# Optimization experiments

Hardware: AMD Instinct MI355X
Metric: run time of the kernel (lower is better)

Reference implementation:

```python
import jax, jax.numpy as jnp
import numpy as np

B, S = 2, 2048          # sequences, tokens per sequence (equal-length varlen batch)
HK, HV = 16, 32         # key heads, value heads (GQA ratio 2)
DK = DV = 128           # head dims (asserted equal in module)
K = 4                   # causal conv kernel width
QKV = HK * DK * 2 + HV * DV  # 8192
CHUNK = 64
EPS = 1e-6


def _causal_conv1d_silu(x, w):
    # x: [B, S, QKV], w: [QKV, K] depthwise causal conv (zero history), then SiLU
    xp = jnp.pad(x, ((0, 0), (K - 1, 0), (0, 0)))
    y = xp[:, 0:S, :] * w[:, 0]
    for j in range(1, K):
        y = y + xp[:, j:j + S, :] * w[:, j]
    return jax.nn.silu(y)


def _l2norm(x):
    return x * jax.lax.rsqrt(jnp.sum(x * x, axis=-1, keepdims=True) + EPS)


def _gdn_forward(mixed_qkv, b, a, conv_weights, dt_bias, alog):
    x = mixed_qkv.reshape(B, S, QKV)
    y = _causal_conv1d_silu(x, conv_weights)
    q = _l2norm(y[..., :HK * DK].reshape(B, S, HK, DK))
    k = _l2norm(y[..., HK * DK:2 * HK * DK].reshape(B, S, HK, DK))
    v = y[..., 2 * HK * DK:].reshape(B, S, HV, DV)
    # fused_gdn_gating: g = -exp(A_log) * softplus(a + dt_bias), beta = sigmoid(b)
    g = (-jnp.exp(alog) * jax.nn.softplus(a + dt_bias)).reshape(B, S, HV)
    beta = jax.nn.sigmoid(b).reshape(B, S, HV)
    r = HV // HK  # GQA: repeat q/k heads to match value heads
    q = jnp.repeat(q, r, axis=2)
    k = jnp.repeat(k, r, axis=2)
    scale = DK ** -0.5

    def tm(t):  # [B,S,...] -> [S//CHUNK, CHUNK, B, ...] (time-major, chunked)
        tt = jnp.moveaxis(t, 1, 0)
        return tt.reshape((S // CHUNK, CHUNK) + tt.shape[1:])

    qs, ks, vs, gs, bs = tm(q), tm(k), tm(v), tm(g), tm(beta)

    def inner(St, inp):
        # St: [B,HV,DK,DV] gated delta-rule state
        qt, kt, vt, gt, bt = inp
        St = St * jnp.exp(gt)[..., None, None]
        pred = jnp.einsum('bhk,bhkv->bhv', kt, St)
        St = St + kt[..., None] * (bt[..., None] * (vt - pred))[..., None, :]
        o = jnp.einsum('bhk,bhkv->bhv', qt * scale, St)
        return St, o

    @jax.checkpoint
    def chunk_step(St, cin):
        return jax.lax.scan(inner, St, cin)

    S0 = jnp.zeros((B, HV, DK, DV), mixed_qkv.dtype)
    _, o = jax.lax.scan(chunk_step, S0, (qs, ks, vs, gs, bs))
    o = o.reshape(S, B, HV, DV)           # [S,B,HV,DV]
    return jnp.moveaxis(o, 0, 1).reshape(B * S, HV, DV)


def setup_inputs() -> dict:
    ks = jax.random.split(jax.random.key(0), 6)
    return {
        'mixed_qkv': jax.random.normal(ks[0], (B * S, QKV), jnp.float32),
        'b': jax.random.normal(ks[1], (B * S, HV), jnp.float32),
        'a': jax.random.normal(ks[2], (B * S, HV), jnp.float32),
        'conv_weights': 0.25 * jax.random.normal(ks[3], (QKV, K), jnp.float32),
        'dt_bias': jax.random.normal(ks[4], (HV,), jnp.float32),
        'alog': jax.random.normal(ks[5], (HV,), jnp.float32),
        'cu_seqlens': jnp.arange(B + 1, dtype=jnp.int32) * S,
    }


def reference(mixed_qkv, b, a, conv_weights, dt_bias, alog, cu_seqlens):
    # cu_seqlens encodes equal-length sequences [0, S, 2S]; math uses the [B,S] reshape
    return _gdn_forward(mixed_qkv, b, a, conv_weights, dt_bias, alog)
```

## Files before the change

### kernel.cpp

```cpp
#include <hip/hip_runtime.h>
#include <hip/hip_bf16.h>


#define B_    2
#define S_    2048
#define HK_   16
#define HV_   32
#define DK_   128
#define QKV_  8192
#define EPS_  1e-6f
#define SCALE_ 0.08838834764831845f
#define CH_   16
#define NCH_  (S_ / CH_)

#define AS_GLOBAL __attribute__((address_space(1)))
#define AS_LDS    __attribute__((address_space(3)))

__device__ __forceinline__ void gload16(const float* src, float* dst) {
    __builtin_amdgcn_global_load_lds((const AS_GLOBAL void*)src,
                                     (AS_LDS void*)dst, 16, 0, 0);
}
__device__ __forceinline__ void gload4(const float* src, float* dst) {
    __builtin_amdgcn_global_load_lds((const AS_GLOBAL void*)src,
                                     (AS_LDS void*)dst, 4, 0, 0);
}

__device__ __forceinline__ float red8(float x) {
    int t;
    t = __builtin_amdgcn_update_dpp(0, __float_as_int(x), 0xB1, 0xF, 0xF, true);
    x += __int_as_float(t);
    t = __builtin_amdgcn_update_dpp(0, __float_as_int(x), 0x4E, 0xF, 0xF, true);
    x += __int_as_float(t);
    t = __builtin_amdgcn_update_dpp(0, __float_as_int(x), 0x141, 0xF, 0xF, true);
    x += __int_as_float(t);
    return x;
}

__global__ __launch_bounds__(256)
void preproc_kernel(const float* __restrict__ x, const float* __restrict__ w,
                    float* __restrict__ Y)
{
    const int seg = blockIdx.x;
    const int bt0 = blockIdx.y * 4;
    const int t0  = bt0 & (S_ - 1);
    const int tid = threadIdx.x;
    const int c0  = seg * 2048 + tid * 8;

    float4 w4[8];
#pragma unroll
    for (int i = 0; i < 8; ++i)
        w4[i] = *reinterpret_cast<const float4*>(&w[(c0 + i) * 4]);

    float h0[8], h1[8], h2[8], cur[8], y[8];

#pragma unroll
    for (int i = 0; i < 8; ++i) { h0[i] = 0.f; h1[i] = 0.f; h2[i] = 0.f; }
    if (t0 >= 3) {
        const float* r0 = &x[(size_t)(bt0 - 3) * QKV_ + c0];
        const float* r1 = &x[(size_t)(bt0 - 2) * QKV_ + c0];
        const float* r2 = &x[(size_t)(bt0 - 1) * QKV_ + c0];
#pragma unroll
        for (int i4 = 0; i4 < 2; ++i4) {
            const float4 a = *reinterpret_cast<const float4*>(r0 + i4 * 4);
            const float4 b = *reinterpret_cast<const float4*>(r1 + i4 * 4);
            const float4 c = *reinterpret_cast<const float4*>(r2 + i4 * 4);
            h0[4*i4+0]=a.x; h0[4*i4+1]=a.y; h0[4*i4+2]=a.z; h0[4*i4+3]=a.w;
            h1[4*i4+0]=b.x; h1[4*i4+1]=b.y; h1[4*i4+2]=b.z; h1[4*i4+3]=b.w;
            h2[4*i4+0]=c.x; h2[4*i4+1]=c.y; h2[4*i4+2]=c.z; h2[4*i4+3]=c.w;
        }
    }

#pragma unroll
    for (int tt = 0; tt < 4; ++tt) {
        const float* rc = &x[(size_t)(bt0 + tt) * QKV_ + c0];
#pragma unroll
        for (int i4 = 0; i4 < 2; ++i4) {
            const float4 a = *reinterpret_cast<const float4*>(rc + i4 * 4);
            cur[4*i4+0]=a.x; cur[4*i4+1]=a.y; cur[4*i4+2]=a.z; cur[4*i4+3]=a.w;
        }
#pragma unroll
        for (int i = 0; i < 8; ++i) {
            float v = h0[i]*w4[i].x + h1[i]*w4[i].y + h2[i]*w4[i].z + cur[i]*w4[i].w;
            y[i] = v / (1.f + expf(-v));
        }
        if (seg < 2) {
            float s = 0.f;
#pragma unroll
            for (int i = 0; i < 8; ++i) s += y[i] * y[i];
#pragma unroll
            for (int off = 8; off >= 1; off >>= 1)
                s += __shfl_xor(s, off, 64);
            float rn = rsqrtf(s + EPS_);
            if (seg == 0) rn *= SCALE_;
#pragma unroll
            for (int i = 0; i < 8; ++i) y[i] *= rn;
        }
        float4* dst = reinterpret_cast<float4*>(&Y[(size_t)(bt0 + tt) * QKV_ + c0]);
        dst[0] = make_float4(y[0], y[1], y[2], y[3]);
        dst[1] = make_float4(y[4], y[5], y[6], y[7]);
#pragma unroll
        for (int i = 0; i < 8; ++i) { h0[i] = h1[i]; h1[i] = h2[i]; h2[i] = cur[i]; }
    }
}

__global__ __launch_bounds__(256)
void gating_kernel(const float* __restrict__ bin, const float* __restrict__ ain,
                   const float* __restrict__ dtb, const float* __restrict__ alg,
                   float2* __restrict__ GB)
{
    const int i = blockIdx.x * 256 + threadIdx.x;
    if (i >= B_ * S_ * HV_) return;
    const int h = i & (HV_ - 1);
    const float av = ain[i] + dtb[h];
    const float sp = (av > 20.f) ? av : log1pf(expf(av));
    GB[i] = make_float2(expf(-expf(alg[h]) * sp), 1.f / (1.f + expf(-bin[i])));
}

__device__ __forceinline__ void lds_load_kqv(const float* __restrict__ Kt,
                                             const float* __restrict__ Qt,
                                             const float* __restrict__ Vt,
                                             int kh, int vloc, int sw,
                                             float (&kf)[16], float (&qf)[16],
                                             float& vv)
{
#pragma unroll
    for (int r = 0; r < 4; ++r) {
        const int idx = r ^ sw;
        const float4 kq = *reinterpret_cast<const float4*>(Kt + kh * 16 + idx * 4);
        const float4 qq = *reinterpret_cast<const float4*>(Qt + kh * 16 + idx * 4);
        kf[4*r+0]=kq.x; kf[4*r+1]=kq.y; kf[4*r+2]=kq.z; kf[4*r+3]=kq.w;
        qf[4*r+0]=qq.x; qf[4*r+1]=qq.y; qf[4*r+2]=qq.z; qf[4*r+3]=qq.w;
    }
    vv = Vt[vloc];
}

__device__ __forceinline__ void step_pair(float (&S)[16],
    const float (&k0)[16], const float (&q0)[16], float v0,
    const float (&k1)[16], const float (&q1)[16], float v1,
    float4 g,
    int kh, float* __restrict__ o0p, float* __restrict__ o1p)
{
    float a0 = 0.f, a1 = 0.f, cc = 0.f, u0 = 0.f,
          u1 = 0.f, w00 = 0.f, w10 = 0.f, w11 = 0.f;
#pragma unroll
    for (int j = 0; j < 16; ++j) {
        a0  += k0[j] * S[j];
        a1  += k1[j] * S[j];
        cc  += k1[j] * k0[j];
        u0  += q0[j] * S[j];
        u1  += q1[j] * S[j];
        w00 += q0[j] * k0[j];
        w10 += q1[j] * k0[j];
        w11 += q1[j] * k1[j];
    }
    a0 = red8(a0);  a1 = red8(a1);  cc = red8(cc);  u0 = red8(u0);
    u1 = red8(u1);  w00 = red8(w00); w10 = red8(w10); w11 = red8(w11);

    const float eg0 = g.x, b0 = g.y, eg1 = g.z, b1 = g.w;
    const float d0   = b0 * (v0 - eg0 * a0);
    const float eg01 = eg0 * eg1;
    const float p1   = fmaf(eg1 * cc, d0, eg01 * a1);
    const float d1   = b1 * (v1 - p1);
    const float o0   = fmaf(w00, d0, eg0 * u0);
    const float o1   = fmaf(w11, d1, fmaf(eg1 * w10, d0, eg01 * u1));
    const float bb   = eg1 * d0;
#pragma unroll
    for (int j = 0; j < 16; ++j)
        S[j] = fmaf(eg01, S[j], fmaf(bb, k0[j], d1 * k1[j]));

    if (kh == 0) { *o0p = o0; *o1p = o1; }
}

__global__ __launch_bounds__(64, 1)
void recur_kernel(const float* __restrict__ Y, const float2* __restrict__ GB,
                  float* __restrict__ out)
{
    const int h    = blockIdx.x;
    const int b    = blockIdx.y;
    const int vs   = blockIdx.z;
    const int hk   = h >> 1;
    const int lane = threadIdx.x;
    const int kh   = lane & 7;
    const int vloc = lane >> 3;
    const int sw   = kh >> 1;

    const int qoff0 = hk * DK_;
    const int koff0 = 2048 + hk * DK_;
    const int voff0 = 4096 + h * DK_ + vs * 8;

    __shared__ __align__(16) float Ksm[2][CH_][128];
    __shared__ __align__(16) float Qsm[2][CH_][128];
    __shared__ __align__(16) float Vsm[2][CH_ * 8];
    __shared__ __align__(16) float Gsm[2][64];

    const float* rowBase = Y + (size_t)(b * S_) * QKV_;
    const float* gflat   = (const float*)(GB + (size_t)(b * S_) * HV_ + h);
    float* obase = out + ((size_t)(b * S_) * HV_ + h) * (size_t)DK_ + vs * 8 + vloc;

    const int tk = lane >> 5;
    const int gr = lane & 31;

    auto issue_chunk = [&](int t0, int bsel) {
#pragma unroll
        for (int i = 0; i < 8; ++i)
            gload16(rowBase + (size_t)(t0 + 2 * i + tk) * QKV_ + koff0 + gr * 4,
                    &Ksm[bsel][2 * i][0]);
#pragma unroll
        for (int i = 0; i < 8; ++i)
            gload16(rowBase + (size_t)(t0 + 2 * i + tk) * QKV_ + qoff0 + gr * 4,
                    &Qsm[bsel][2 * i][0]);
#pragma unroll
        for (int i = 0; i < 2; ++i)
            gload4(rowBase + (size_t)(t0 + i * 8 + (lane >> 3)) * QKV_
                           + voff0 + (lane & 7),
                   &Vsm[bsel][i * 64]);
        gload4(gflat + (size_t)(t0 + ((lane >> 1) & 15)) * (HV_ * 2) + (lane & 1),
               &Gsm[bsel][0]);
    };

    float S[16];
#pragma unroll
    for (int j = 0; j < 16; ++j) S[j] = 0.f;

    issue_chunk(0, 0);
    issue_chunk(CH_, 1);
    asm volatile("s_waitcnt vmcnt(19)" ::: "memory");

    float k0A[16], q0A[16], k1A[16], q1A[16], v0A, v1A;
    float k0B[16], q0B[16], k1B[16], q1B[16], v0B, v1B;
    float4 gA, gB4;

    for (int c = 0; c < NCH_; ++c) {
        const int bsel = c & 1;
        const int t0   = c * CH_;
        const float (*Kc)[128] = Ksm[bsel];
        const float (*Qc)[128] = Qsm[bsel];
        const float* Vc = Vsm[bsel];
        const float* Gc = Gsm[bsel];

        lds_load_kqv(Kc[0], Qc[0], Vc + 0,  kh, vloc, sw, k0A, q0A, v0A);
        lds_load_kqv(Kc[1], Qc[1], Vc + 8,  kh, vloc, sw, k1A, q1A, v1A);
        gA = *reinterpret_cast<const float4*>(Gc + 0);
        lds_load_kqv(Kc[2], Qc[2], Vc + 16, kh, vloc, sw, k0B, q0B, v0B);
        lds_load_kqv(Kc[3], Qc[3], Vc + 24, kh, vloc, sw, k1B, q1B, v1B);
        gB4 = *reinterpret_cast<const float4*>(Gc + 4);

#pragma unroll
        for (int pp = 0; pp < CH_ / 2; pp += 2) {
            step_pair(S, k0A, q0A, v0A, k1A, q1A, v1A, gA, kh,
                      obase + (size_t)(t0 + 2 * pp)     * (HV_ * DK_),
                      obase + (size_t)(t0 + 2 * pp + 1) * (HV_ * DK_));
            if (pp + 2 < CH_ / 2) {
                const int ta = 2 * (pp + 2);
                lds_load_kqv(Kc[ta],     Qc[ta],     Vc + ta * 8,
                             kh, vloc, sw, k0A, q0A, v0A);
                lds_load_kqv(Kc[ta + 1], Qc[ta + 1], Vc + (ta + 1) * 8,
                             kh, vloc, sw, k1A, q1A, v1A);
                gA = *reinterpret_cast<const float4*>(Gc + 2 * ta);
            }
            __builtin_amdgcn_sched_barrier(0);
            step_pair(S, k0B, q0B, v0B, k1B, q1B, v1B, gB4, kh,
                      obase + (size_t)(t0 + 2 * pp + 2) * (HV_ * DK_),
                      obase + (size_t)(t0 + 2 * pp + 3) * (HV_ * DK_));
            if (pp + 3 < CH_ / 2) {
                const int tb = 2 * (pp + 3);
                lds_load_kqv(Kc[tb],     Qc[tb],     Vc + tb * 8,
                             kh, vloc, sw, k0B, q0B, v0B);
                lds_load_kqv(Kc[tb + 1], Qc[tb + 1], Vc + (tb + 1) * 8,
                             kh, vloc, sw, k1B, q1B, v1B);
                gB4 = *reinterpret_cast<const float4*>(Gc + 2 * tb);
            }
        }

        const int tn = (c + 2 < NCH_) ? (c + 2) * CH_ : (NCH_ - 1) * CH_;
        issue_chunk(tn, bsel);
        asm volatile("s_waitcnt vmcnt(35)" ::: "memory");
    }
}

__global__ __launch_bounds__(128)
void gdn_prefill_fallback(const float* __restrict__ xqkv, const float* __restrict__ bin,
                          const float* __restrict__ ain, const float* __restrict__ wconv,
                          const float* __restrict__ dtb, const float* __restrict__ alg,
                          float* __restrict__ out)
{
    const int h = blockIdx.x, b = blockIdx.y;
    const int hk = h >> 1;
    const int tid = threadIdx.x, lane = tid & 63, wid = tid >> 6;
    __shared__ __align__(16) float ks[DK_];
    __shared__ __align__(16) float qs[DK_];
    __shared__ float redq[2], redk[2];
    const int qc = hk * DK_ + tid, kc = HK_ * DK_ + hk * DK_ + tid,
              vc = 2 * HK_ * DK_ + h * DK_ + tid;
    float wq[4], wk[4], wv[4];
#pragma unroll
    for (int j = 0; j < 4; ++j) {
        wq[j] = wconv[qc*4+j]; wk[j] = wconv[kc*4+j]; wv[j] = wconv[vc*4+j];
    }
    const float nea = -expf(alg[h]), dbi = dtb[h];
    float hq0=0,hq1=0,hq2=0,hk0=0,hk1=0,hk2=0,hv0=0,hv1=0,hv2=0;
    float Sr[DK_];
#pragma unroll
    for (int k = 0; k < DK_; ++k) Sr[k] = 0.f;
    const size_t row0 = (size_t)b * S_;
    for (int t = 0; t < S_; ++t) {
        const size_t row = row0 + t, xb = row * QKV_;
        const float xq = xqkv[xb+qc], xk = xqkv[xb+kc], xv = xqkv[xb+vc];
        float yq = hq0*wq[0]+hq1*wq[1]+hq2*wq[2]+xq*wq[3];
        float yk = hk0*wk[0]+hk1*wk[1]+hk2*wk[2]+xk*wk[3];
        float yv = hv0*wv[0]+hv1*wv[1]+hv2*wv[2]+xv*wv[3];
        hq0=hq1;hq1=hq2;hq2=xq; hk0=hk1;hk1=hk2;hk2=xk; hv0=hv1;hv1=hv2;hv2=xv;
        yq = yq/(1.f+expf(-yq)); yk = yk/(1.f+expf(-yk)); yv = yv/(1.f+expf(-yv));
        float sq = yq*yq, sk = yk*yk;
#pragma unroll
        for (int off = 32; off >= 1; off >>= 1) {
            sq += __shfl_xor(sq, off, 64); sk += __shfl_xor(sk, off, 64);
        }
        if (lane == 0) { redq[wid] = sq; redk[wid] = sk; }
        __syncthreads();
        const float qn = yq * rsqrtf(redq[0]+redq[1]+EPS_) * SCALE_;
        const float kn = yk * rsqrtf(redk[0]+redk[1]+EPS_);
        ks[tid] = kn; qs[tid] = qn;
        const size_t rab = row * HV_ + h;
        const float av = ain[rab] + dbi;
        const float sp = (av > 20.f) ? av : log1pf(expf(av));
        const float eg = expf(nea * sp);
        const float beta = 1.f/(1.f+expf(-bin[rab]));
        __syncthreads();
        float pred = 0.f;
#pragma unroll
        for (int k4 = 0; k4 < DK_/4; ++k4) {
            const float4 kv = *reinterpret_cast<const float4*>(&ks[k4*4]);
            float s;
            s = Sr[4*k4+0]*eg; Sr[4*k4+0]=s; pred += kv.x*s;
            s = Sr[4*k4+1]*eg; Sr[4*k4+1]=s; pred += kv.y*s;
            s = Sr[4*k4+2]*eg; Sr[4*k4+2]=s; pred += kv.z*s;
            s = Sr[4*k4+3]*eg; Sr[4*k4+3]=s; pred += kv.w*s;
        }
        const float delta = beta * (yv - pred);
        float o = 0.f;
#pragma unroll
        for (int k4 = 0; k4 < DK_/4; ++k4) {
            const float4 kv = *reinterpret_cast<const float4*>(&ks[k4*4]);
            const float4 qv = *reinterpret_cast<const float4*>(&qs[k4*4]);
            float s;
            s = Sr[4*k4+0]+kv.x*delta; Sr[4*k4+0]=s; o += qv.x*s;
            s = Sr[4*k4+1]+kv.y*delta; Sr[4*k4+1]=s; o += qv.y*s;
            s = Sr[4*k4+2]+kv.z*delta; Sr[4*k4+2]=s; o += qv.z*s;
            s = Sr[4*k4+3]+kv.w*delta; Sr[4*k4+3]=s; o += qv.w*s;
        }
        out[rab * DK_ + tid] = o;
    }
}

extern "C" void kernel_launch(void* const* d_in, const int* in_sizes, int n_in,
                              void* d_out, int out_size, void* d_ws, size_t ws_size,
                              hipStream_t stream) {
    const float* xqkv  = (const float*)d_in[0];
    const float* bin   = (const float*)d_in[1];
    const float* ain   = (const float*)d_in[2];
    const float* wconv = (const float*)d_in[3];
    const float* dtb   = (const float*)d_in[4];
    const float* alg   = (const float*)d_in[5];
    float* out = (float*)d_out;

    const size_t Y_BYTES = (size_t)B_ * S_ * QKV_ * 4;
    const size_t G_BYTES = (size_t)B_ * S_ * HV_ * 8;
    const size_t NEEDED  = Y_BYTES + G_BYTES;

    if (ws_size >= NEEDED) {
        float*  Y  = (float*)d_ws;
        float2* GB = (float2*)((char*)d_ws + Y_BYTES);

        preproc_kernel<<<dim3(4, B_ * S_ / 4), 256, 0, stream>>>(xqkv, wconv, Y);
        gating_kernel<<<dim3((B_ * S_ * HV_ + 255) / 256), 256, 0, stream>>>(
            bin, ain, dtb, alg, GB);
        recur_kernel<<<dim3(HV_, B_, 16), 64, 0, stream>>>(Y, GB, out);
    } else {
        gdn_prefill_fallback<<<dim3(HV_, B_), 128, 0, stream>>>(
            xqkv, bin, ain, wconv, dtb, alg, out);
    }
}
```

Baseline: 827.2 us.

## Split recurrence state across 16 lanes and double the value-column grid

Each wavefront now owns 4 value columns instead of 8, with 16 lanes each holding 8 key rows of the state instead of 8 lanes holding 16. The grid's z dimension doubles to 32, the chunk size drops to 8, and the DPP reduction gains a fourth stage to cover 16 lanes. The aim is to shorten the serial per-token dependency chain and put more wavefronts on the GPU, since the recurrence is latency-bound. In exchange, every block reloads the full K/Q rows for fewer outputs, doubling redundant loads, and each dot product pays an extra reduction step.

Result: slower. 1.116 ms (+34.9%).

```diff
diff --git a/kernel.cpp b/kernel.cpp
--- a/kernel.cpp
+++ b/kernel.cpp
@@ -10,7 +10,7 @@
 #define QKV_  8192
 #define EPS_  1e-6f
 #define SCALE_ 0.08838834764831845f
-#define CH_   16
+#define CH_   8
 #define NCH_  (S_ / CH_)
 
 #define AS_GLOBAL __attribute__((address_space(1)))
@@ -25,7 +25,7 @@
                                      (AS_LDS void*)dst, 4, 0, 0);
 }
 
-__device__ __forceinline__ float red8(float x) {
+__device__ __forceinline__ float red16(float x) {
     int t;
     t = __builtin_amdgcn_update_dpp(0, __float_as_int(x), 0xB1, 0xF, 0xF, true);
     x += __int_as_float(t);
@@ -33,6 +33,8 @@
     x += __int_as_float(t);
     t = __builtin_amdgcn_update_dpp(0, __float_as_int(x), 0x141, 0xF, 0xF, true);
     x += __int_as_float(t);
+    t = __builtin_amdgcn_update_dpp(0, __float_as_int(x), 0x140, 0xF, 0xF, true);
+    x += __int_as_float(t);
     return x;
 }
 
@@ -116,34 +118,34 @@
     GB[i] = make_float2(expf(-expf(alg[h]) * sp), 1.f / (1.f + expf(-bin[i])));
 }
 
-__device__ __forceinline__ void lds_load_kqv(const float* __restrict__ Kt,
-                                             const float* __restrict__ Qt,
-                                             const float* __restrict__ Vt,
-                                             int kh, int vloc, int sw,
-                                             float (&kf)[16], float (&qf)[16],
-                                             float& vv)
-{
-#pragma unroll
-    for (int r = 0; r < 4; ++r) {
+__device__ __forceinline__ void lds_load_kqv8(const float* __restrict__ Kt,
+                                              const float* __restrict__ Qt,
+                                              const float* __restrict__ Vt,
+                                              int kh16, int vloc, int sw,
+                                              float (&kf)[8], float (&qf)[8],
+                                              float& vv)
+{
+#pragma unroll
+    for (int r = 0; r < 2; ++r) {
         const int idx = r ^ sw;
-        const float4 kq = *reinterpret_cast<const float4*>(Kt + kh * 16 + idx * 4);
-        const float4 qq = *reinterpret_cast<const float4*>(Qt + kh * 16 + idx * 4);
+        const float4 kq = *reinterpret_cast<const float4*>(Kt + kh16 * 8 + idx * 4);
+        const float4 qq = *reinterpret_cast<const float4*>(Qt + kh16 * 8 + idx * 4);
         kf[4*r+0]=kq.x; kf[4*r+1]=kq.y; kf[4*r+2]=kq.z; kf[4*r+3]=kq.w;
         qf[4*r+0]=qq.x; qf[4*r+1]=qq.y; qf[4*r+2]=qq.z; qf[4*r+3]=qq.w;
     }
     vv = Vt[vloc];
 }
 
-__device__ __forceinline__ void step_pair(float (&S)[16],
-    const float (&k0)[16], const float (&q0)[16], float v0,
-    const float (&k1)[16], const float (&q1)[16], float v1,
+__device__ __forceinline__ void step_pair(float (&S)[8],
+    const float (&k0)[8], const float (&q0)[8], float v0,
+    const float (&k1)[8], const float (&q1)[8], float v1,
     float4 g,
-    int kh, float* __restrict__ o0p, float* __restrict__ o1p)
+    int kh16, float* __restrict__ o0p, float* __restrict__ o1p)
 {
     float a0 = 0.f, a1 = 0.f, cc = 0.f, u0 = 0.f,
           u1 = 0.f, w00 = 0.f, w10 = 0.f, w11 = 0.f;
 #pragma unroll
-    for (int j = 0; j < 16; ++j) {
+    for (int j = 0; j < 8; ++j) {
         a0  += k0[j] * S[j];
         a1  += k1[j] * S[j];
         cc  += k1[j] * k0[j];
@@ -153,8 +155,8 @@
         w10 += q1[j] * k0[j];
         w11 += q1[j] * k1[j];
     }
-    a0 = red8(a0);  a1 = red8(a1);  cc = red8(cc);  u0 = red8(u0);
-    u1 = red8(u1);  w00 = red8(w00); w10 = red8(w10); w11 = red8(w11);
+    a0 = red16(a0);  a1 = red16(a1);  cc = red16(cc);  u0 = red16(u0);
+    u1 = red16(u1);  w00 = red16(w00); w10 = red16(w10); w11 = red16(w11);
 
     const float eg0 = g.x, b0 = g.y, eg1 = g.z, b1 = g.w;
     const float d0   = b0 * (v0 - eg0 * a0);
@@ -165,13 +167,13 @@
     const float o1   = fmaf(w11, d1, fmaf(eg1 * w10, d0, eg01 * u1));
     const float bb   = eg1 * d0;
 #pragma unroll
-    for (int j = 0; j < 16; ++j)
+    for (int j = 0; j < 8; ++j)
         S[j] = fmaf(eg01, S[j], fmaf(bb, k0[j], d1 * k1[j]));
 
-    if (kh == 0) { *o0p = o0; *o1p = o1; }
-}
-
-__global__ __launch_bounds__(64, 1)
+    if (kh16 == 0) { *o0p = o0; *o1p = o1; }
+}
+
+__global__ __launch_bounds__(64, 2)
 void recur_kernel(const float* __restrict__ Y, const float2* __restrict__ GB,
                   float* __restrict__ out)
 {
@@ -180,54 +182,51 @@
     const int vs   = blockIdx.z;
     const int hk   = h >> 1;
     const int lane = threadIdx.x;
-    const int kh   = lane & 7;
-    const int vloc = lane >> 3;
-    const int sw   = kh >> 1;
+    const int kh16 = lane & 15;
+    const int vloc = lane >> 4;
+    const int sw   = (kh16 >> 2) & 1;
 
     const int qoff0 = hk * DK_;
     const int koff0 = 2048 + hk * DK_;
-    const int voff0 = 4096 + h * DK_ + vs * 8;
+    const int voff0 = 4096 + h * DK_ + vs * 4;
 
     __shared__ __align__(16) float Ksm[2][CH_][128];
     __shared__ __align__(16) float Qsm[2][CH_][128];
-    __shared__ __align__(16) float Vsm[2][CH_ * 8];
+    __shared__ __align__(16) float Vsm[2][64];
     __shared__ __align__(16) float Gsm[2][64];
 
     const float* rowBase = Y + (size_t)(b * S_) * QKV_;
     const float* gflat   = (const float*)(GB + (size_t)(b * S_) * HV_ + h);
-    float* obase = out + ((size_t)(b * S_) * HV_ + h) * (size_t)DK_ + vs * 8 + vloc;
-
-    const int tk = lane >> 5;
-    const int gr = lane & 31;
+    float* obase = out + ((size_t)(b * S_) * HV_ + h) * (size_t)DK_ + vs * 4 + vloc;
 
     auto issue_chunk = [&](int t0, int bsel) {
 #pragma unroll
-        for (int i = 0; i < 8; ++i)
-            gload16(rowBase + (size_t)(t0 + 2 * i + tk) * QKV_ + koff0 + gr * 4,
+        for (int i = 0; i < 4; ++i)
+            gload16(rowBase + (size_t)(t0 + 2 * i + (lane >> 5)) * QKV_
+                            + koff0 + (lane & 31) * 4,
                     &Ksm[bsel][2 * i][0]);
 #pragma unroll
-        for (int i = 0; i < 8; ++i)
-            gload16(rowBase + (size_t)(t0 + 2 * i + tk) * QKV_ + qoff0 + gr * 4,
+        for (int i = 0; i < 4; ++i)
+            gload16(rowBase + (size_t)(t0 + 2 * i + (lane >> 5)) * QKV_
+                            + qoff0 + (lane & 31) * 4,
                     &Qsm[bsel][2 * i][0]);
-#pragma unroll
-        for (int i = 0; i < 2; ++i)
-            gload4(rowBase + (size_t)(t0 + i * 8 + (lane >> 3)) * QKV_
-                           + voff0 + (lane & 7),
-                   &Vsm[bsel][i * 64]);
-        gload4(gflat + (size_t)(t0 + ((lane >> 1) & 15)) * (HV_ * 2) + (lane & 1),
+        gload4(rowBase + (size_t)(t0 + ((lane >> 2) & 7)) * QKV_
+                       + voff0 + (lane & 3),
+               &Vsm[bsel][0]);
+        gload4(gflat + (size_t)(t0 + ((lane >> 1) & 7)) * (HV_ * 2) + (lane & 1),
                &Gsm[bsel][0]);
     };
 
-    float S[16];
-#pragma unroll
-    for (int j = 0; j < 16; ++j) S[j] = 0.f;
+    float S[8];
+#pragma unroll
+    for (int j = 0; j < 8; ++j) S[j] = 0.f;
 
     issue_chunk(0, 0);
     issue_chunk(CH_, 1);
-    asm volatile("s_waitcnt vmcnt(19)" ::: "memory");
-
-    float k0A[16], q0A[16], k1A[16], q1A[16], v0A, v1A;
-    float k0B[16], q0B[16], k1B[16], q1B[16], v0B, v1B;
+    asm volatile("s_waitcnt vmcnt(10)" ::: "memory");
+
+    float k0A[8], q0A[8], k1A[8], q1A[8], v0A, v1A;
+    float k0B[8], q0B[8], k1B[8], q1B[8], v0B, v1B;
     float4 gA, gB4;
 
     for (int c = 0; c < NCH_; ++c) {
@@ -238,43 +237,43 @@
         const float* Vc = Vsm[bsel];
         const float* Gc = Gsm[bsel];
 
-        lds_load_kqv(Kc[0], Qc[0], Vc + 0,  kh, vloc, sw, k0A, q0A, v0A);
-        lds_load_kqv(Kc[1], Qc[1], Vc + 8,  kh, vloc, sw, k1A, q1A, v1A);
+        lds_load_kqv8(Kc[0], Qc[0], Vc + 0,  kh16, vloc, sw, k0A, q0A, v0A);
+        lds_load_kqv8(Kc[1], Qc[1], Vc + 4,  kh16, vloc, sw, k1A, q1A, v1A);
         gA = *reinterpret_cast<const float4*>(Gc + 0);
-        lds_load_kqv(Kc[2], Qc[2], Vc + 16, kh, vloc, sw, k0B, q0B, v0B);
-        lds_load_kqv(Kc[3], Qc[3], Vc + 24, kh, vloc, sw, k1B, q1B, v1B);
+        lds_load_kqv8(Kc[2], Qc[2], Vc + 8,  kh16, vloc, sw, k0B, q0B, v0B);
+        lds_load_kqv8(Kc[3], Qc[3], Vc + 12, kh16, vloc, sw, k1B, q1B, v1B);
         gB4 = *reinterpret_cast<const float4*>(Gc + 4);
 
 #pragma unroll
         for (int pp = 0; pp < CH_ / 2; pp += 2) {
-            step_pair(S, k0A, q0A, v0A, k1A, q1A, v1A, gA, kh,
+            step_pair(S, k0A, q0A, v0A, k1A, q1A, v1A, gA, kh16,
                       obase + (size_t)(t0 + 2 * pp)     * (HV_ * DK_),
                       obase + (size_t)(t0 + 2 * pp + 1) * (HV_ * DK_));
             if (pp + 2 < CH_ / 2) {
                 const int ta = 2 * (pp + 2);
-                lds_load_kqv(Kc[ta],     Qc[ta],     Vc + ta * 8,
-                             kh, vloc, sw, k0A, q0A, v0A);
-                lds_load_kqv(Kc[ta + 1], Qc[ta + 1], Vc + (ta + 1) * 8,
-                             kh, vloc, sw, k1A, q1A, v1A);
+                lds_load_kqv8(Kc[ta],     Qc[ta],     Vc + ta * 4,
+                              kh16, vloc, sw, k0A, q0A, v0A);
+                lds_load_kqv8(Kc[ta + 1], Qc[ta + 1], Vc + (ta + 1) * 4,
+                              kh16, vloc, sw, k1A, q1A, v1A);
                 gA = *reinterpret_cast<const float4*>(Gc + 2 * ta);
             }
             __builtin_amdgcn_sched_barrier(0);
-            step_pair(S, k0B, q0B, v0B, k1B, q1B, v1B, gB4, kh,
+            step_pair(S, k0B, q0B, v0B, k1B, q1B, v1B, gB4, kh16,
                       obase + (size_t)(t0 + 2 * pp + 2) * (HV_ * DK_),
                       obase + (size_t)(t0 + 2 * pp + 3) * (HV_ * DK_));
             if (pp + 3 < CH_ / 2) {
                 const int tb = 2 * (pp + 3);
-                lds_load_kqv(Kc[tb],     Qc[tb],     Vc + tb * 8,
-                             kh, vloc, sw, k0B, q0B, v0B);
-                lds_load_kqv(Kc[tb + 1], Qc[tb + 1], Vc + (tb + 1) * 8,
-                             kh, vloc, sw, k1B, q1B, v1B);
+                lds_load_kqv8(Kc[tb],     Qc[tb],     Vc + tb * 4,
+                              kh16, vloc, sw, k0B, q0B, v0B);
+                lds_load_kqv8(Kc[tb + 1], Qc[tb + 1], Vc + (tb + 1) * 4,
+                              kh16, vloc, sw, k1B, q1B, v1B);
                 gB4 = *reinterpret_cast<const float4*>(Gc + 2 * tb);
             }
         }
 
         const int tn = (c + 2 < NCH_) ? (c + 2) * CH_ : (NCH_ - 1) * CH_;
         issue_chunk(tn, bsel);
-        asm volatile("s_waitcnt vmcnt(35)" ::: "memory");
+        asm volatile("s_waitcnt vmcnt(18)" ::: "memory");
     }
 }
 
@@ -375,7 +374,7 @@
         preproc_kernel<<<dim3(4, B_ * S_ / 4), 256, 0, stream>>>(xqkv, wconv, Y);
         gating_kernel<<<dim3((B_ * S_ * HV_ + 255) / 256), 256, 0, stream>>>(
             bin, ain, dtb, alg, GB);
-        recur_kernel<<<dim3(HV_, B_, 16), 64, 0, stream>>>(Y, GB, out);
+        recur_kernel<<<dim3(HV_, B_, 32), 64, 0, stream>>>(Y, GB, out);
     } else {
         gdn_prefill_fallback<<<dim3(HV_, B_), 128, 0, stream>>>(
             xqkv, bin, ain, wconv, dtb, alg, out);
```

## Precompute per-pair k/q dot products in a separate kernel for the recurrence

Applied to the files above, without the earlier changes.

Adds a dot_kernel that computes the state-independent dot products (k1·k0, q0·k0, q1·k0, q1·k1) for each timestep pair once per key head. The recurrence kernel then loads them through LDS instead of computing and reducing them in every one of its 16 value-slice blocks and both GQA value heads. This halves the FMA and cross-lane reduction work on the serial critical path, at the cost of an extra launch, an extra workspace buffer and one more async load per chunk.

After: 696.1 us. 15.8% less time.

```diff
diff --git a/kernel.cpp b/kernel.cpp
--- a/kernel.cpp
+++ b/kernel.cpp
@@ -116,6 +116,39 @@
     GB[i] = make_float2(expf(-expf(alg[h]) * sp), 1.f / (1.f + expf(-bin[i])));
 }
 
+__global__ __launch_bounds__(256)
+void dot_kernel(const float* __restrict__ Y, float4* __restrict__ CD)
+{
+    const int lane = threadIdx.x & 63;
+    const int i    = blockIdx.x * 4 + (threadIdx.x >> 6);
+    const int p    = i & (S_ / 2 - 1);
+    const int bh   = i >> 10;
+    const int hk   = bh & (HK_ - 1);
+    const int b    = bh >> 4;
+    const int ch   = lane * 2;
+    const size_t r0 = (size_t)(b * S_ + 2 * p) * QKV_;
+    const int koff = 2048 + hk * DK_ + ch;
+    const int qoff = hk * DK_ + ch;
+
+    const float2 k0 = *reinterpret_cast<const float2*>(&Y[r0 + koff]);
+    const float2 q0 = *reinterpret_cast<const float2*>(&Y[r0 + qoff]);
+    const float2 k1 = *reinterpret_cast<const float2*>(&Y[r0 + QKV_ + koff]);
+    const float2 q1 = *reinterpret_cast<const float2*>(&Y[r0 + QKV_ + qoff]);
+
+    float cc  = k1.x * k0.x + k1.y * k0.y;
+    float w00 = q0.x * k0.x + q0.y * k0.y;
+    float w10 = q1.x * k0.x + q1.y * k0.y;
+    float w11 = q1.x * k1.x + q1.y * k1.y;
+#pragma unroll
+    for (int off = 32; off >= 1; off >>= 1) {
+        cc  += __shfl_xor(cc,  off, 64);
+        w00 += __shfl_xor(w00, off, 64);
+        w10 += __shfl_xor(w10, off, 64);
+        w11 += __shfl_xor(w11, off, 64);
+    }
+    if (lane == 0) CD[i] = make_float4(cc, w00, w10, w11);
+}
+
 __device__ __forceinline__ void lds_load_kqv(const float* __restrict__ Kt,
                                              const float* __restrict__ Qt,
                                              const float* __restrict__ Vt,
@@ -138,25 +171,21 @@
     const float (&k0)[16], const float (&q0)[16], float v0,
     const float (&k1)[16], const float (&q1)[16], float v1,
     float4 g,
+    float4 cd,
     int kh, float* __restrict__ o0p, float* __restrict__ o1p)
 {
-    float a0 = 0.f, a1 = 0.f, cc = 0.f, u0 = 0.f,
-          u1 = 0.f, w00 = 0.f, w10 = 0.f, w11 = 0.f;
+    float a0 = 0.f, a1 = 0.f, u0 = 0.f, u1 = 0.f;
 #pragma unroll
     for (int j = 0; j < 16; ++j) {
-        a0  += k0[j] * S[j];
-        a1  += k1[j] * S[j];
-        cc  += k1[j] * k0[j];
-        u0  += q0[j] * S[j];
-        u1  += q1[j] * S[j];
-        w00 += q0[j] * k0[j];
-        w10 += q1[j] * k0[j];
-        w11 += q1[j] * k1[j];
-    }
-    a0 = red8(a0);  a1 = red8(a1);  cc = red8(cc);  u0 = red8(u0);
-    u1 = red8(u1);  w00 = red8(w00); w10 = red8(w10); w11 = red8(w11);
+        a0 += k0[j] * S[j];
+        a1 += k1[j] * S[j];
+        u0 += q0[j] * S[j];
+        u1 += q1[j] * S[j];
+    }
+    a0 = red8(a0);  a1 = red8(a1);  u0 = red8(u0);  u1 = red8(u1);
 
     const float eg0 = g.x, b0 = g.y, eg1 = g.z, b1 = g.w;
+    const float cc = cd.x, w00 = cd.y, w10 = cd.z, w11 = cd.w;
     const float d0   = b0 * (v0 - eg0 * a0);
     const float eg01 = eg0 * eg1;
     const float p1   = fmaf(eg1 * cc, d0, eg01 * a1);
@@ -173,7 +202,7 @@
 
 __global__ __launch_bounds__(64, 1)
 void recur_kernel(const float* __restrict__ Y, const float2* __restrict__ GB,
-                  float* __restrict__ out)
+                  const float* __restrict__ CDg, float* __restrict__ out)
 {
     const int h    = blockIdx.x;
     const int b    = blockIdx.y;
@@ -192,9 +221,11 @@
     __shared__ __align__(16) float Qsm[2][CH_][128];
     __shared__ __align__(16) float Vsm[2][CH_ * 8];
     __shared__ __align__(16) float Gsm[2][64];
+    __shared__ __align__(16) float CDsm[2][64];
 
     const float* rowBase = Y + (size_t)(b * S_) * QKV_;
     const float* gflat   = (const float*)(GB + (size_t)(b * S_) * HV_ + h);
+    const float* cdflat  = CDg + (size_t)(b * HK_ + hk) * (S_ / 2) * 4;
     float* obase = out + ((size_t)(b * S_) * HV_ + h) * (size_t)DK_ + vs * 8 + vloc;
 
     const int tk = lane >> 5;
@@ -216,6 +247,8 @@
                    &Vsm[bsel][i * 64]);
         gload4(gflat + (size_t)(t0 + ((lane >> 1) & 15)) * (HV_ * 2) + (lane & 1),
                &Gsm[bsel][0]);
+        gload4(cdflat + (size_t)(t0 / 2) * 4 + (lane & 31),
+               &CDsm[bsel][0]);
     };
 
     float S[16];
@@ -224,30 +257,33 @@
 
     issue_chunk(0, 0);
     issue_chunk(CH_, 1);
-    asm volatile("s_waitcnt vmcnt(19)" ::: "memory");
+    asm volatile("s_waitcnt vmcnt(20)" ::: "memory");
 
     float k0A[16], q0A[16], k1A[16], q1A[16], v0A, v1A;
     float k0B[16], q0B[16], k1B[16], q1B[16], v0B, v1B;
-    float4 gA, gB4;
+    float4 gA, gB4, cdA, cdB;
 
     for (int c = 0; c < NCH_; ++c) {
         const int bsel = c & 1;
         const int t0   = c * CH_;
         const float (*Kc)[128] = Ksm[bsel];
         const float (*Qc)[128] = Qsm[bsel];
-        const float* Vc = Vsm[bsel];
-        const float* Gc = Gsm[bsel];
+        const float* Vc  = Vsm[bsel];
+        const float* Gc  = Gsm[bsel];
+        const float* CDc = CDsm[bsel];
 
         lds_load_kqv(Kc[0], Qc[0], Vc + 0,  kh, vloc, sw, k0A, q0A, v0A);
         lds_load_kqv(Kc[1], Qc[1], Vc + 8,  kh, vloc, sw, k1A, q1A, v1A);
-        gA = *reinterpret_cast<const float4*>(Gc + 0);
+        gA  = *reinterpret_cast<const float4*>(Gc + 0);
+        cdA = *reinterpret_cast<const float4*>(CDc + 0);
         lds_load_kqv(Kc[2], Qc[2], Vc + 16, kh, vloc, sw, k0B, q0B, v0B);
         lds_load_kqv(Kc[3], Qc[3], Vc + 24, kh, vloc, sw, k1B, q1B, v1B);
         gB4 = *reinterpret_cast<const float4*>(Gc + 4);
+        cdB = *reinterpret_cast<const float4*>(CDc + 4);
 
 #pragma unroll
         for (int pp = 0; pp < CH_ / 2; pp += 2) {
-            step_pair(S, k0A, q0A, v0A, k1A, q1A, v1A, gA, kh,
+            step_pair(S, k0A, q0A, v0A, k1A, q1A, v1A, gA, cdA, kh,
                       obase + (size_t)(t0 + 2 * pp)     * (HV_ * DK_),
                       obase + (size_t)(t0 + 2 * pp + 1) * (HV_ * DK_));
             if (pp + 2 < CH_ / 2) {
@@ -256,10 +292,11 @@
                              kh, vloc, sw, k0A, q0A, v0A);
                 lds_load_kqv(Kc[ta + 1], Qc[ta + 1], Vc + (ta + 1) * 8,
                              kh, vloc, sw, k1A, q1A, v1A);
-                gA = *reinterpret_cast<const float4*>(Gc + 2 * ta);
+                gA  = *reinterpret_cast<const float4*>(Gc + 2 * ta);
+                cdA = *reinterpret_cast<const float4*>(CDc + 4 * (pp + 2));
             }
             __builtin_amdgcn_sched_barrier(0);
-            step_pair(S, k0B, q0B, v0B, k1B, q1B, v1B, gB4, kh,
+            step_pair(S, k0B, q0B, v0B, k1B, q1B, v1B, gB4, cdB, kh,
                       obase + (size_t)(t0 + 2 * pp + 2) * (HV_ * DK_),
                       obase + (size_t)(t0 + 2 * pp + 3) * (HV_ * DK_));
             if (pp + 3 < CH_ / 2) {
@@ -269,12 +306,13 @@
                 lds_load_kqv(Kc[tb + 1], Qc[tb + 1], Vc + (tb + 1) * 8,
                              kh, vloc, sw, k1B, q1B, v1B);
                 gB4 = *reinterpret_cast<const float4*>(Gc + 2 * tb);
+                cdB = *reinterpret_cast<const float4*>(CDc + 4 * (pp + 3));
             }
         }
 
         const int tn = (c + 2 < NCH_) ? (c + 2) * CH_ : (NCH_ - 1) * CH_;
         issue_chunk(tn, bsel);
-        asm volatile("s_waitcnt vmcnt(35)" ::: "memory");
+        asm volatile("s_waitcnt vmcnt(36)" ::: "memory");
     }
 }
 
@@ -364,18 +402,22 @@
     const float* alg   = (const float*)d_in[5];
     float* out = (float*)d_out;
 
-    const size_t Y_BYTES = (size_t)B_ * S_ * QKV_ * 4;
-    const size_t G_BYTES = (size_t)B_ * S_ * HV_ * 8;
-    const size_t NEEDED  = Y_BYTES + G_BYTES;
+    const size_t Y_BYTES  = (size_t)B_ * S_ * QKV_ * 4;
+    const size_t G_BYTES  = (size_t)B_ * S_ * HV_ * 8;
+    const size_t CD_BYTES = (size_t)B_ * HK_ * (S_ / 2) * 16;
+    const size_t NEEDED   = Y_BYTES + G_BYTES + CD_BYTES;
 
     if (ws_size >= NEEDED) {
         float*  Y  = (float*)d_ws;
         float2* GB = (float2*)((char*)d_ws + Y_BYTES);
+        float*  CD = (float*)((char*)d_ws + Y_BYTES + G_BYTES);
 
         preproc_kernel<<<dim3(4, B_ * S_ / 4), 256, 0, stream>>>(xqkv, wconv, Y);
         gating_kernel<<<dim3((B_ * S_ * HV_ + 255) / 256), 256, 0, stream>>>(
             bin, ain, dtb, alg, GB);
-        recur_kernel<<<dim3(HV_, B_, 16), 64, 0, stream>>>(Y, GB, out);
+        dot_kernel<<<dim3(B_ * HK_ * (S_ / 2) / 4), 256, 0, stream>>>(
+            Y, (float4*)CD);
+        recur_kernel<<<dim3(HV_, B_, 16), 64, 0, stream>>>(Y, GB, CD, out);
     } else {
         gdn_prefill_fallback<<<dim3(HV_, B_), 128, 0, stream>>>(
             xqkv, bin, ain, wconv, dtb, alg, out);
```
